# Optimization experiments

Hardware: AMD Instinct MI355X
Metric: run time of the kernel (lower is better)

## Reference

```python
import jax, jax.numpy as jnp
import numpy as np

B, T, C, H = 2, 2048, 1024, 16
N = C // H
TM_DIM, TD_DIM = 32, 64
EPS = 1e-5 * 8 ** 2  # GroupNorm eps from the module


def setup_inputs() -> dict:
    key = jax.random.key(0)
    ks = jax.random.split(key, 16)
    nrm = lambda k, shp, s: jax.random.normal(k, shp, dtype=jnp.float32) * s
    uni = lambda k, shp, a: jax.random.uniform(k, shp, jnp.float32, -a, a)
    ddd = (jnp.arange(C, dtype=jnp.float32) / C).reshape(1, 1, C)
    return {
        "x": nrm(ks[0], (B, T, C), 1.0),
        "time_maa_x": 1.0 - ddd ** 0.5,
        "time_maa_w": 1.0 - ddd ** 0.5,
        "time_maa_k": 1.0 - ddd ** 0.5,
        "time_maa_v": 1.0 - (ddd ** 0.5 + 0.15),
        "time_maa_r": 1.0 - ddd ** 0.25,
        "time_maa_g": 1.0 - ddd ** 0.25,
        "time_maa_w1": uni(ks[1], (C, 5 * TM_DIM), 1e-4),
        "time_maa_w2": uni(ks[2], (5, TM_DIM, C), 1e-4),
        "time_decay": jnp.linspace(-6.0, -1.0, C).astype(jnp.float32).reshape(1, 1, C),
        "time_decay_w1": uni(ks[3], (C, TD_DIM), 1e-4),
        "time_decay_w2": uni(ks[4], (TD_DIM, C), 1e-4),
        "time_faaaa": nrm(ks[5], (H, N), 0.1),
        "W_r": nrm(ks[6], (C, C), C ** -0.5),
        "W_k": nrm(ks[7], (C, C), C ** -0.5),
        "W_v": nrm(ks[8], (C, C), C ** -0.5),
        "W_g": nrm(ks[9], (C, C), C ** -0.5),
        "W_o": nrm(ks[10], (C, C), C ** -0.5),
        "ln_w": jnp.ones((C,), jnp.float32),
        "ln_b": jnp.zeros((C,), jnp.float32),
    }


def _forward(x, tmx, tmw, tmk, tmv, tmr, tmg, maa_w1, maa_w2, tdecay, td_w1,
             td_w2, u, Wr, Wk, Wv, Wg, Wo, ln_w, ln_b):
    Bq, Tq, Cq = x.shape
    # time_shift: x[t-1] with zero at t=0
    xx = jnp.concatenate([jnp.zeros_like(x[:, :1]), x[:, :-1]], axis=1) - x
    xxx = x + xx * tmx
    t5 = jnp.tanh(xxx @ maa_w1).reshape(Bq, Tq, 5, TM_DIM)
    m = jnp.einsum('btfe,fec->fbtc', t5, maa_w2)  # [5,B,T,C] data-dependent mix
    xw = x + xx * (tmw + m[0])
    xk = x + xx * (tmk + m[1])
    xv = x + xx * (tmv + m[2])
    xr = x + xx * (tmr + m[3])
    xg = x + xx * (tmg + m[4])
    r = xr @ Wr
    k = xk @ Wk
    v = xv @ Wv
    g = jax.nn.silu(xg @ Wg)
    w = tdecay + jnp.tanh(xw @ td_w1) @ td_w2          # [B,T,C] log-log decay
    decay = jnp.exp(-jnp.exp(w))                        # in (0,1)
    to_tbhn = lambda a: a.reshape(Bq, Tq, H, N).transpose(1, 0, 2, 3)
    rT, kT, vT, dT = (to_tbhn(a) for a in (r, k, v, decay))

    def step(S, inp):  # S: [B,H,N,N] (key_dim i, value_dim j)
        r_t, k_t, v_t, d_t = inp
        kv = k_t[..., :, None] * v_t[..., None, :]
        y = jnp.einsum('bhi,bhij->bhj', r_t, S + u[None, :, :, None] * kv)
        return d_t[..., None] * S + kv, y

    S0 = jnp.zeros((Bq, H, N, N), x.dtype)
    _, ys = jax.lax.scan(step, S0, (rT, kT, vT, dT))
    y = ys.transpose(1, 0, 2, 3).reshape(Bq, Tq, Cq)
    # GroupNorm with H groups over channels
    yh = y.reshape(Bq, Tq, H, N)
    mu = yh.mean(-1, keepdims=True)
    var = yh.var(-1, keepdims=True)
    yn = (yh - mu) / jnp.sqrt(var + EPS)
    yn = (yn * ln_w.reshape(H, N) + ln_b.reshape(H, N)).reshape(Bq, Tq, Cq)
    return (yn * g) @ Wo


def reference(x, time_maa_x, time_maa_w, time_maa_k, time_maa_v, time_maa_r,
              time_maa_g, time_maa_w1, time_maa_w2, time_decay, time_decay_w1,
              time_decay_w2, time_faaaa, W_r, W_k, W_v, W_g, W_o, ln_w, ln_b):
    return _forward(x, time_maa_x, time_maa_w, time_maa_k, time_maa_v,
                    time_maa_r, time_maa_g, time_maa_w1, time_maa_w2,
                    time_decay, time_decay_w1, time_decay_w2, time_faaaa,
                    W_r, W_k, W_v, W_g, W_o, ln_w, ln_b)
```

## Files before the change

kernel.cpp:

```cpp
#include <hip/hip_runtime.h>
#include <hip/hip_bf16.h>
#include <cstdint>
#include <cstddef>

#define B_ 2
#define T_ 2048
#define C_ 1024
#define H_ 16
#define NCH 32
#define CHL 64

typedef unsigned short ushort_t;
typedef __bf16 bf16x8 __attribute__((ext_vector_type(8)));
typedef float f32x4 __attribute__((ext_vector_type(4)));

__device__ __forceinline__ ushort_t f2bf(float f) {
  union { float f; uint32_t u; } x; x.f = f;
  uint32_t r = x.u + 0x7fffu + ((x.u >> 16) & 1u);
  return (ushort_t)(r >> 16);
}
__device__ __forceinline__ float bf2f(ushort_t h) {
  union { uint32_t u; float f; } x; x.u = (uint32_t)h << 16; return x.f;
}

__device__ __forceinline__ void gload16(const void* g, void* l) {
  __builtin_amdgcn_global_load_lds(
      (const __attribute__((address_space(1))) void*)g,
      (__attribute__((address_space(3))) void*)l, 16, 0, 0);
}

#define FENCE() asm volatile("" ::: "memory")
#define BAR() do { FENCE(); __builtin_amdgcn_s_barrier(); FENCE(); } while (0)

__device__ __forceinline__ void stb(ushort_t* tile, int row, int col, ushort_t v) {
  *(ushort_t*)((char*)tile + row * 128 + ((col * 2) ^ ((row & 7) << 4))) = v;
}
__device__ __forceinline__ bf16x8 ldb(const ushort_t* tile, int row, int kbyte) {
  return *(const bf16x8*)((const char*)tile + row * 128 + (kbyte ^ ((row & 7) << 4)));
}

struct TDesc { const float* src; ushort_t* dst; int R, Cc, Cpad; };
struct TArgs { TDesc d[9]; };

__global__ __launch_bounds__(256) void transpose_cvt(TArgs args) {
  TDesc D = args.d[blockIdx.z];
  int c0 = blockIdx.x * 32, r0 = blockIdx.y * 32;
  if (c0 >= D.Cpad || r0 >= D.R) return;
  __shared__ float tile[32][33];
  int tx = threadIdx.x & 31, ty = threadIdx.x >> 5;
#pragma unroll
  for (int i = 0; i < 32; i += 8) {
    int r = r0 + ty + i, c = c0 + tx;
    tile[ty + i][tx] = (r < D.R && c < D.Cc) ? D.src[(size_t)r * D.Cc + c] : 0.f;
  }
  __syncthreads();
#pragma unroll
  for (int i = 0; i < 32; i += 8) {
    int c = c0 + ty + i, r = r0 + tx;
    if (c < D.Cpad && r < D.R) D.dst[(size_t)c * D.R + r] = f2bf(tile[tx][ty + i]);
  }
}

__global__ __launch_bounds__(256) void prep_kernel(
    const float* __restrict__ x, const float* __restrict__ tmx,
    float* __restrict__ xx, ushort_t* __restrict__ xxx) {
  size_t idx = ((size_t)blockIdx.x * 256 + threadIdx.x) * 4;
  int tt = (int)((idx >> 10) & (T_ - 1));
  int c = (int)(idx & (C_ - 1));
  float4 xv = *(const float4*)&x[idx];
  float4 xp;
  if (tt == 0) { xp.x = xp.y = xp.z = xp.w = 0.f; }
  else xp = *(const float4*)&x[idx - C_];
  float4 tm = *(const float4*)&tmx[c];
  float4 d;
  d.x = xp.x - xv.x; d.y = xp.y - xv.y; d.z = xp.z - xv.z; d.w = xp.w - xv.w;
  *(float4*)&xx[idx] = d;
  xxx[idx + 0] = f2bf(xv.x + d.x * tm.x);
  xxx[idx + 1] = f2bf(xv.y + d.y * tm.y);
  xxx[idx + 2] = f2bf(xv.z + d.z * tm.z);
  xxx[idx + 3] = f2bf(xv.w + d.w * tm.w);
}

template <int EPI>
__global__ __launch_bounds__(256) void gemm_bt(
    const ushort_t* __restrict__ A, int lda,
    const ushort_t* __restrict__ Bt, int ldb,
    void* __restrict__ Cp, int ldc, int K,
    const float* __restrict__ aux2) {
  __shared__ ushort_t sA[128 * 32];
  __shared__ ushort_t sB[128 * 32];
  const int t = threadIdx.x;
  const int l = t & 63;
  const int w = t >> 6;
  const int wm = w >> 1, wn = w & 1;
  const int m0 = blockIdx.x * 128, n0 = blockIdx.y * 128;
  const int lr = l & 15;
  const int lk = (l >> 4) * 8;

  f32x4 acc[4][4] = {};

  for (int kt = 0; kt < K; kt += 32) {
    __syncthreads();
#pragma unroll
    for (int it = 0; it < 2; ++it) {
      int cbase = it * 256 + w * 64;
      int ca = cbase + l;
      int row = ca >> 2, kc = ca & 3;
      gload16(A + (size_t)(m0 + row) * lda + kt + kc * 8, (char*)sA + (size_t)cbase * 16);
      gload16(Bt + (size_t)(n0 + row) * ldb + kt + kc * 8, (char*)sB + (size_t)cbase * 16);
    }
    __syncthreads();
    bf16x8 af[4], bfr[4];
#pragma unroll
    for (int mi = 0; mi < 4; ++mi)
      af[mi] = *(const bf16x8*)&sA[(wm * 64 + mi * 16 + lr) * 32 + lk];
#pragma unroll
    for (int ni = 0; ni < 4; ++ni)
      bfr[ni] = *(const bf16x8*)&sB[(wn * 64 + ni * 16 + lr) * 32 + lk];
#pragma unroll
    for (int mi = 0; mi < 4; ++mi)
#pragma unroll
      for (int ni = 0; ni < 4; ++ni)
        acc[mi][ni] = __builtin_amdgcn_mfma_f32_16x16x32_bf16(af[mi], bfr[ni], acc[mi][ni], 0, 0, 0);
  }
#pragma unroll
  for (int mi = 0; mi < 4; ++mi) {
#pragma unroll
    for (int ni = 0; ni < 4; ++ni) {
      int col = n0 + wn * 64 + ni * 16 + lr;
#pragma unroll
      for (int r = 0; r < 4; ++r) {
        int row = m0 + wm * 64 + mi * 16 + (l >> 4) * 4 + r;
        float v = acc[mi][ni][r];
        size_t idx = (size_t)row * ldc + col;
        if constexpr (EPI == 4) {
          ((float*)Cp)[idx] = __expf(aux2[col] + v);
        } else {
          ((float*)Cp)[idx] = v;
        }
      }
    }
  }
}

__global__ __launch_bounds__(256) void gemm_bt32(
    const ushort_t* __restrict__ A, int lda,
    const ushort_t* __restrict__ Bt, int ldb,
    ushort_t* __restrict__ Cp, int ldc, int K) {
  __shared__ ushort_t sA[32 * 32];
  __shared__ ushort_t sB[128 * 32];
  const int t = threadIdx.x;
  const int l = t & 63;
  const int w = t >> 6;
  const int m0 = blockIdx.x * 32, n0 = blockIdx.y * 128;
  const int lr = l & 15, lk = (l >> 4) * 8;

  f32x4 acc[2][2] = {};
  for (int kt = 0; kt < K; kt += 32) {
    __syncthreads();
    if (t < 128) {
      int row = t >> 2, kc = t & 3;
      gload16(A + (size_t)(m0 + row) * lda + kt + kc * 8, (char*)sA + t * 16);
    }
#pragma unroll
    for (int it = 0; it < 2; ++it) {
      int ca = it * 256 + t;
      int row = ca >> 2, kc = ca & 3;
      gload16(Bt + (size_t)(n0 + row) * ldb + kt + kc * 8,
              (char*)sB + it * 4096 + w * 1024);
    }
    __syncthreads();
    bf16x8 af[2], bfr[2];
#pragma unroll
    for (int mi = 0; mi < 2; ++mi)
      af[mi] = *(const bf16x8*)&sA[(mi * 16 + lr) * 32 + lk];
#pragma unroll
    for (int ni = 0; ni < 2; ++ni)
      bfr[ni] = *(const bf16x8*)&sB[(w * 32 + ni * 16 + lr) * 32 + lk];
#pragma unroll
    for (int mi = 0; mi < 2; ++mi)
#pragma unroll
      for (int ni = 0; ni < 2; ++ni)
        acc[mi][ni] = __builtin_amdgcn_mfma_f32_16x16x32_bf16(af[mi], bfr[ni], acc[mi][ni], 0, 0, 0);
  }
#pragma unroll
  for (int mi = 0; mi < 2; ++mi)
#pragma unroll
    for (int ni = 0; ni < 2; ++ni) {
      int col = n0 + w * 32 + ni * 16 + lr;
#pragma unroll
      for (int r = 0; r < 4; ++r) {
        int row = m0 + mi * 16 + (l >> 4) * 4 + r;
        Cp[(size_t)row * ldc + col] = f2bf(tanhf(acc[mi][ni][r]));
      }
    }
}

struct PDesc { const ushort_t* A; const ushort_t* Bt; void* C; int epi; };
struct PArgs { PDesc d[4]; };

__global__ __launch_bounds__(512, 1) void gemm_proj256(PArgs args) {
  PDesc D = args.d[blockIdx.z];
  __shared__ ushort_t sMem[2][2][4][4096];
  const int tid = threadIdx.x;
  const int w = tid >> 6, l = tid & 63;
  const int wm = w >> 2, wn = w & 3;
  const int lr = l & 15, hi4 = l >> 4;
  const int m0 = blockIdx.x * 256, n0 = blockIdx.y * 256;

  const int srow = tid >> 3;
  const int scol = (((tid & 7) ^ (srow & 7)) << 3);
  const ushort_t* Abase = D.A + (size_t)(m0 + srow) * C_ + scol;
  const ushort_t* Bbase = D.Bt + (size_t)(n0 + srow) * C_ + scol;
  const int dst16 = tid * 16;

  f32x4 acc[8][4] = {};
  bf16x8 bfr[2][4];

#define STG_A(db, unit, kt) \
  gload16(Abase + (size_t)(unit) * 64 * C_ + (kt), (char*)&sMem[db][0][unit][0] + dst16)
#define STG_B(db, unit, kt) \
  gload16(Bbase + (size_t)(unit) * 64 * C_ + (kt), (char*)&sMem[db][1][unit][0] + dst16)

#define LDA_(b, p, i, kk)                                                      \
  (*(const bf16x8*)((const char*)&sMem[b][0][wm * 2 + ((p) >> 1)][0] +         \
                    (((2 * (p) + (i)) & 3) * 16 + lr) * 128 +                  \
                    ((((kk)*4 + hi4) ^ (lr & 7)) << 4)))
#define LDB_(b, ni, kk)                                                        \
  (*(const bf16x8*)((const char*)&sMem[b][1][wn][0] +                          \
                    ((ni)*16 + lr) * 128 + ((((kk)*4 + hi4) ^ (lr & 7)) << 4)))

#define PH(b, p, STAGES, VM)                                                   \
  do {                                                                         \
    bf16x8 a00, a10, a01, a11;                                                 \
    if ((p) == 0) {                                                            \
      _Pragma("unroll") for (int kk = 0; kk < 2; ++kk)                         \
      _Pragma("unroll") for (int ni = 0; ni < 4; ++ni)                         \
        bfr[kk][ni] = LDB_(b, ni, kk);                                         \
    }                                                                          \
    a00 = LDA_(b, p, 0, 0); a10 = LDA_(b, p, 1, 0);                            \
    a01 = LDA_(b, p, 0, 1); a11 = LDA_(b, p, 1, 1);                            \
    STAGES;                                                                    \
    VM;                                                                        \
    BAR();                                                                     \
    asm volatile("s_waitcnt lgkmcnt(0)" ::: "memory");                         \
    __builtin_amdgcn_sched_barrier(0);                                         \
    __builtin_amdgcn_s_setprio(1);                                             \
    _Pragma("unroll") for (int ni = 0; ni < 4; ++ni) {                         \
      acc[2 * (p)][ni] = __builtin_amdgcn_mfma_f32_16x16x32_bf16(              \
          a00, bfr[0][ni], acc[2 * (p)][ni], 0, 0, 0);                         \
      acc[2 * (p) + 1][ni] = __builtin_amdgcn_mfma_f32_16x16x32_bf16(          \
          a10, bfr[0][ni], acc[2 * (p) + 1][ni], 0, 0, 0);                     \
      acc[2 * (p)][ni] = __builtin_amdgcn_mfma_f32_16x16x32_bf16(              \
          a01, bfr[1][ni], acc[2 * (p)][ni], 0, 0, 0);                         \
      acc[2 * (p) + 1][ni] = __builtin_amdgcn_mfma_f32_16x16x32_bf16(          \
          a11, bfr[1][ni], acc[2 * (p) + 1][ni], 0, 0, 0);                     \
    }                                                                          \
    __builtin_amdgcn_s_setprio(0);                                             \
    BAR();                                                                     \
  } while (0)

#define TILE(b, kt1, kt2)                                                      \
  do {                                                                         \
    PH(b, 0, { STG_A((b) ^ 1, 1, kt1); STG_A((b) ^ 1, 3, kt1); }, );           \
    PH(b, 1, { STG_B(b, 0, kt2); STG_B(b, 1, kt2); },                          \
       asm volatile("s_waitcnt vmcnt(10)" ::: "memory"));                      \
    PH(b, 2, { STG_B(b, 2, kt2); STG_B(b, 3, kt2); }, );                       \
    PH(b, 3, { STG_A(b, 0, kt2); STG_A(b, 2, kt2); },                          \
       asm volatile("s_waitcnt vmcnt(8)" ::: "memory"));                       \
  } while (0)

  STG_B(0, 0, 0);  STG_B(0, 1, 0);
  STG_B(0, 2, 0);  STG_B(0, 3, 0);
  STG_A(0, 0, 0);  STG_A(0, 2, 0);
  STG_A(0, 1, 0);  STG_A(0, 3, 0);
  STG_B(1, 0, 64); STG_B(1, 1, 64);
  STG_B(1, 2, 64); STG_B(1, 3, 64);
  STG_A(1, 0, 64); STG_A(1, 2, 64);
  asm volatile("s_waitcnt vmcnt(8)" ::: "memory");
  BAR();

#pragma unroll 1
  for (int j = 0; j < 16; j += 2) {
    int ka1 = ((j + 1) & 15) * 64, ka2 = ((j + 2) & 15) * 64;
    int kb1 = ((j + 2) & 15) * 64, kb2 = ((j + 3) & 15) * 64;
    TILE(0, ka1, ka2);
    TILE(1, kb1, kb2);
  }
  asm volatile("s_waitcnt vmcnt(0)" ::: "memory");

  const int epi = D.epi;
#pragma unroll
  for (int mi = 0; mi < 8; ++mi)
#pragma unroll
    for (int ni = 0; ni < 4; ++ni) {
      int col = n0 + wn * 64 + ni * 16 + lr;
#pragma unroll
      for (int r = 0; r < 4; ++r) {
        int row = m0 + wm * 128 + mi * 16 + hi4 * 4 + r;
        float v = acc[mi][ni][r];
        size_t idx = (size_t)row * C_ + col;
        if (epi == 2) {
          v = v / (1.f + __expf(-v));
          ((ushort_t*)D.C)[idx] = f2bf(v);
        } else {
          ((float*)D.C)[idx] = v;
        }
      }
    }
#undef TILE
#undef PH
#undef LDB_
#undef LDA_
#undef STG_B
#undef STG_A
}

struct MixArgs { const float* tm[5]; ushort_t* dst[5]; };

__global__ __launch_bounds__(256) void fused_mix(
    const float* __restrict__ x, const float* __restrict__ xx,
    const ushort_t* __restrict__ t5, const ushort_t* __restrict__ w2t,
    MixArgs margs) {
  __shared__ float xs[64 * 128];
  __shared__ float xxs[64 * 128];
  __shared__ ushort_t sA[64 * 32];
  __shared__ ushort_t sB[128 * 32];
  const int t = threadIdx.x;
  const int l = t & 63;
  const int w = t >> 6;
  const int wm = w >> 1, wn = w & 1;
  const int m0 = blockIdx.x * 64, n0 = blockIdx.y * 128;
  const int lr = l & 15;
  const int lk = (l >> 4) * 8;

#pragma unroll
  for (int it = 0; it < 8; ++it) {
    int row = it * 8 + (t >> 5);
    int c16 = t & 31;
    gload16(x + (size_t)(m0 + row) * C_ + n0 + c16 * 4, (char*)xs + row * 512 + c16 * 16);
    gload16(xx + (size_t)(m0 + row) * C_ + n0 + c16 * 4, (char*)xxs + row * 512 + c16 * 16);
  }

  for (int f = 0; f < 5; ++f) {
    __syncthreads();
    {
      int row = t >> 2, c8 = t & 3;
      gload16(t5 + (size_t)(m0 + row) * 256 + f * 32 + c8 * 8, (char*)sA + t * 16);
    }
#pragma unroll
    for (int it = 0; it < 2; ++it) {
      int row = it * 64 + (t >> 2), c8 = t & 3;
      gload16(w2t + (size_t)(n0 + row) * 160 + f * 32 + c8 * 8,
              (char*)sB + it * 4096 + t * 16);
    }
    __syncthreads();
    bf16x8 af[2], bfr[4];
#pragma unroll
    for (int mi = 0; mi < 2; ++mi)
      af[mi] = *(const bf16x8*)&sA[(wm * 32 + mi * 16 + lr) * 32 + lk];
#pragma unroll
    for (int ni = 0; ni < 4; ++ni)
      bfr[ni] = *(const bf16x8*)&sB[(wn * 64 + ni * 16 + lr) * 32 + lk];
    f32x4 acc[2][4] = {};
#pragma unroll
    for (int mi = 0; mi < 2; ++mi)
#pragma unroll
      for (int ni = 0; ni < 4; ++ni)
        acc[mi][ni] = __builtin_amdgcn_mfma_f32_16x16x32_bf16(af[mi], bfr[ni], acc[mi][ni], 0, 0, 0);
    const float* tmf = margs.tm[f];
    ushort_t* dst = margs.dst[f];
#pragma unroll
    for (int mi = 0; mi < 2; ++mi) {
#pragma unroll
      for (int ni = 0; ni < 4; ++ni) {
        int cl = wn * 64 + ni * 16 + lr;
        int col = n0 + cl;
        float tmv = tmf[col];
#pragma unroll
        for (int r = 0; r < 4; ++r) {
          int rl = wm * 32 + mi * 16 + (l >> 4) * 4 + r;
          int row = m0 + rl;
          float xv = xs[rl * 128 + cl];
          float xxv = xxs[rl * 128 + cl];
          dst[(size_t)row * C_ + col] = f2bf(xv + xxv * (tmv + acc[mi][ni][r]));
        }
      }
    }
  }
}

__global__ __launch_bounds__(256) void chunk_local(
    const float* __restrict__ rx, const float* __restrict__ kx,
    const float* __restrict__ vx, const float* __restrict__ lamx,
    const float* __restrict__ u, float* __restrict__ Mt,
    float* __restrict__ aLg, ushort_t* __restrict__ rAg,
    float* __restrict__ yo) {
  int c = blockIdx.x, bh = blockIdx.y;
  int b = bh >> 4, h = bh & 15;
  __shared__ ushort_t sRA[64 * 64], sKA[64 * 64], sKh[64 * 64], sKl[64 * 64],
                      sVh[64 * 64], sVl[64 * 64], sP[64 * 64];
  __shared__ float qsum[4][64];
  __shared__ float ruk[64];
  const int tid = threadIdx.x;
  const int i = tid & 63;
  const int q = tid >> 6;
  size_t base = ((size_t)b * T_ + (size_t)c * CHL) * C_ + h * 64;
  size_t cb = ((size_t)c * 32 + bh);

  float lam[16];
  float run = 0.f;
#pragma unroll
  for (int s = 0; s < 16; ++s) {
    lam[s] = lamx[base + (size_t)(q * 16 + s) * C_ + i];
    run += lam[s];
  }
  qsum[q][i] = run;
  __syncthreads();
  float pre = 0.f, ct = 0.f;
#pragma unroll
  for (int qq = 0; qq < 4; ++qq) {
    float vq = qsum[qq][i];
    ct += vq;
    if (qq < q) pre += vq;
  }
  float uu = u[h * 64 + i];
  float ci = pre;
#pragma unroll
  for (int s = 0; s < 16; ++s) {
    int t = q * 16 + s;
    ci += lam[s];
    float cl = ci - lam[s];
    size_t o = base + (size_t)t * C_ + i;
    float rv = rx[o], kv = kx[o], vv = vx[o];
    ushort_t ra = f2bf(rv * __expf(-cl));
    stb(sRA, t, i, ra);
    rAg[cb * 4096 + t * 64 + i] = ra;
    stb(sKA, t, i, f2bf(kv * __expf(ci)));
    float kal = kv * __expf(ci - ct);
    ushort_t khv = f2bf(kal);
    stb(sKh, i, t, khv);
    stb(sKl, i, t, f2bf(kal - bf2f(khv)));
    ushort_t vhv = f2bf(vv);
    stb(sVh, i, t, vhv);
    stb(sVl, i, t, f2bf(vv - bf2f(vhv)));
    float rr = rv * uu * kv;
#pragma unroll
    for (int m = 32; m; m >>= 1) rr += __shfl_xor(rr, m);
    if (i == 0) ruk[t] = rr;
  }
  if (q == 0) aLg[cb * 64 + i] = __expf(-ct);
  __syncthreads();

  const int l = tid & 63, w = tid >> 6;
  const int wm = w >> 1, wn = w & 1;
  const int lr = l & 15, hi4 = l >> 4;

  {
    f32x4 accP[2][2] = {};
#pragma unroll
    for (int kk = 0; kk < 2; ++kk) {
      bf16x8 af[2], bf_[2];
#pragma unroll
      for (int mi = 0; mi < 2; ++mi) af[mi] = ldb(sRA, wm * 32 + mi * 16 + lr, kk * 64 + hi4 * 16);
#pragma unroll
      for (int ni = 0; ni < 2; ++ni) bf_[ni] = ldb(sKA, wn * 32 + ni * 16 + lr, kk * 64 + hi4 * 16);
#pragma unroll
      for (int mi = 0; mi < 2; ++mi)
#pragma unroll
        for (int ni = 0; ni < 2; ++ni)
          accP[mi][ni] = __builtin_amdgcn_mfma_f32_16x16x32_bf16(af[mi], bf_[ni], accP[mi][ni], 0, 0, 0);
    }
#pragma unroll
    for (int mi = 0; mi < 2; ++mi)
#pragma unroll
      for (int ni = 0; ni < 2; ++ni)
#pragma unroll
        for (int r = 0; r < 4; ++r) {
          int tl = wm * 32 + mi * 16 + hi4 * 4 + r, sl = wn * 32 + ni * 16 + lr;
          float v = accP[mi][ni][r];
          v = sl < tl ? v : (sl == tl ? ruk[tl] : 0.f);
          stb(sP, tl, sl, f2bf(v));
        }
  }
  __syncthreads();

  f32x4 accY[2][2] = {}, accM[2][2] = {};
#pragma unroll
  for (int kk = 0; kk < 2; ++kk) {
    bf16x8 pa[2], vhA[2], vlA[2], vhB[2], vlB[2], khB[2], klB[2];
#pragma unroll
    for (int mi = 0; mi < 2; ++mi) {
      int rw = wm * 32 + mi * 16 + lr;
      pa[mi] = ldb(sP, rw, kk * 64 + hi4 * 16);
      vhA[mi] = ldb(sVh, rw, kk * 64 + hi4 * 16);
      vlA[mi] = ldb(sVl, rw, kk * 64 + hi4 * 16);
    }
#pragma unroll
    for (int ni = 0; ni < 2; ++ni) {
      int rw = wn * 32 + ni * 16 + lr;
      vhB[ni] = ldb(sVh, rw, kk * 64 + hi4 * 16);
      vlB[ni] = ldb(sVl, rw, kk * 64 + hi4 * 16);
      khB[ni] = ldb(sKh, rw, kk * 64 + hi4 * 16);
      klB[ni] = ldb(sKl, rw, kk * 64 + hi4 * 16);
    }
#pragma unroll
    for (int mi = 0; mi < 2; ++mi)
#pragma unroll
      for (int ni = 0; ni < 2; ++ni) {
        accY[mi][ni] = __builtin_amdgcn_mfma_f32_16x16x32_bf16(pa[mi], vhB[ni], accY[mi][ni], 0, 0, 0);
        accY[mi][ni] = __builtin_amdgcn_mfma_f32_16x16x32_bf16(pa[mi], vlB[ni], accY[mi][ni], 0, 0, 0);
        accM[mi][ni] = __builtin_amdgcn_mfma_f32_16x16x32_bf16(vhA[mi], khB[ni], accM[mi][ni], 0, 0, 0);
        accM[mi][ni] = __builtin_amdgcn_mfma_f32_16x16x32_bf16(vhA[mi], klB[ni], accM[mi][ni], 0, 0, 0);
        accM[mi][ni] = __builtin_amdgcn_mfma_f32_16x16x32_bf16(vlA[mi], khB[ni], accM[mi][ni], 0, 0, 0);
      }
  }
#pragma unroll
  for (int mi = 0; mi < 2; ++mi)
#pragma unroll
    for (int ni = 0; ni < 2; ++ni)
#pragma unroll
      for (int r = 0; r < 4; ++r) {
        int rw = wm * 32 + mi * 16 + hi4 * 4 + r;
        int cw = wn * 32 + ni * 16 + lr;
        yo[base + (size_t)rw * C_ + cw] = accY[mi][ni][r];
        Mt[cb * 4096 + rw * 64 + cw] = accM[mi][ni][r];
      }
}

__global__ __launch_bounds__(256) void combine2(
    const float* __restrict__ Mt, const float* __restrict__ aLg,
    ushort_t* __restrict__ S0h, ushort_t* __restrict__ S0l) {
  int bh = blockIdx.x >> 2;
  int ij = ((blockIdx.x & 3) * 256 + threadIdx.x) * 4;
  int i = ij & 63;
  float4 s = {0.f, 0.f, 0.f, 0.f};
  for (int c = 0; c < NCH; ++c) {
    size_t o = ((size_t)c * 32 + bh) * 4096 + ij;
    float4 m = *(const float4*)&Mt[o];
    float4 p = *(const float4*)&aLg[((size_t)c * 32 + bh) * 64 + i];
    ushort4 hi, lo;
    hi.x = f2bf(s.x); lo.x = f2bf(s.x - bf2f(hi.x));
    hi.y = f2bf(s.y); lo.y = f2bf(s.y - bf2f(hi.y));
    hi.z = f2bf(s.z); lo.z = f2bf(s.z - bf2f(hi.z));
    hi.w = f2bf(s.w); lo.w = f2bf(s.w - bf2f(hi.w));
    *(ushort4*)&S0h[o] = hi;
    *(ushort4*)&S0l[o] = lo;
    s.x = p.x * s.x + m.x; s.y = p.y * s.y + m.y;
    s.z = p.z * s.z + m.z; s.w = p.w * s.w + m.w;
  }
}

__global__ __launch_bounds__(256) void inter_gn(
    const ushort_t* __restrict__ rAg, const ushort_t* __restrict__ S0h,
    const ushort_t* __restrict__ S0l, const float* __restrict__ yin,
    const ushort_t* __restrict__ gx, const float* __restrict__ lnw,
    const float* __restrict__ lnb, ushort_t* __restrict__ Z) {
  int c = blockIdx.x, bh = blockIdx.y;
  int b = bh >> 4, h = bh & 15;
  __shared__ ushort_t sRA[64 * 64], sSh[64 * 64], sSl[64 * 64];
  __shared__ float st[64][2][2];
  const int tid = threadIdx.x;
  size_t cb = ((size_t)c * 32 + bh) * 4096;
#pragma unroll
  for (int it = 0; it < 2; ++it) {
    int lb = tid * 32 + it * 16;
    int row = lb >> 7, wi = lb & 127;
    int so = row * 128 + (wi ^ ((row & 7) << 4));
    *(uint4*)((char*)sRA + so) = *(const uint4*)((const char*)(rAg + cb) + lb);
    *(uint4*)((char*)sSh + so) = *(const uint4*)((const char*)(S0h + cb) + lb);
    *(uint4*)((char*)sSl + so) = *(const uint4*)((const char*)(S0l + cb) + lb);
  }
  const int l = tid & 63, w = tid >> 6;
  const int wm = w >> 1, wn = w & 1;
  const int lr = l & 15, hi4 = l >> 4;
  size_t base = ((size_t)b * T_ + (size_t)c * CHL) * C_ + h * 64;

  f32x4 acc[2][2];
#pragma unroll
  for (int mi = 0; mi < 2; ++mi)
#pragma unroll
    for (int ni = 0; ni < 2; ++ni)
#pragma unroll
      for (int r = 0; r < 4; ++r)
        acc[mi][ni][r] = yin[base + (size_t)(wm * 32 + mi * 16 + hi4 * 4 + r) * C_ +
                             wn * 32 + ni * 16 + lr];
  __syncthreads();
#pragma unroll
  for (int kk = 0; kk < 2; ++kk) {
    bf16x8 af[2], bh_[2], bl_[2];
#pragma unroll
    for (int mi = 0; mi < 2; ++mi) af[mi] = ldb(sRA, wm * 32 + mi * 16 + lr, kk * 64 + hi4 * 16);
#pragma unroll
    for (int ni = 0; ni < 2; ++ni) {
      bh_[ni] = ldb(sSh, wn * 32 + ni * 16 + lr, kk * 64 + hi4 * 16);
      bl_[ni] = ldb(sSl, wn * 32 + ni * 16 + lr, kk * 64 + hi4 * 16);
    }
#pragma unroll
    for (int mi = 0; mi < 2; ++mi)
#pragma unroll
      for (int ni = 0; ni < 2; ++ni) {
        acc[mi][ni] = __builtin_amdgcn_mfma_f32_16x16x32_bf16(af[mi], bh_[ni], acc[mi][ni], 0, 0, 0);
        acc[mi][ni] = __builtin_amdgcn_mfma_f32_16x16x32_bf16(af[mi], bl_[ni], acc[mi][ni], 0, 0, 0);
      }
  }
#pragma unroll
  for (int mi = 0; mi < 2; ++mi)
#pragma unroll
    for (int r = 0; r < 4; ++r) {
      int row = wm * 32 + mi * 16 + hi4 * 4 + r;
      float s1 = acc[mi][0][r] + acc[mi][1][r];
      float s2 = acc[mi][0][r] * acc[mi][0][r] + acc[mi][1][r] * acc[mi][1][r];
#pragma unroll
      for (int m = 1; m < 16; m <<= 1) { s1 += __shfl_xor(s1, m); s2 += __shfl_xor(s2, m); }
      if (lr == 0) { st[row][wn][0] = s1; st[row][wn][1] = s2; }
    }
  __syncthreads();
#pragma unroll
  for (int mi = 0; mi < 2; ++mi)
#pragma unroll
    for (int ni = 0; ni < 2; ++ni)
#pragma unroll
      for (int r = 0; r < 4; ++r) {
        int row = wm * 32 + mi * 16 + hi4 * 4 + r;
        int jl = wn * 32 + ni * 16 + lr;
        float S1 = st[row][0][0] + st[row][1][0];
        float S2 = st[row][0][1] + st[row][1][1];
        float mu = S1 * (1.f / 64.f);
        float var = S2 * (1.f / 64.f) - mu * mu;
        float rs = rsqrtf(var + 6.4e-4f);
        int col = h * 64 + jl;
        size_t o = base + (size_t)row * C_ + jl;
        float yn = (acc[mi][ni][r] - mu) * rs * lnw[col] + lnb[col];
        Z[o] = f2bf(yn * bf2f(gx[o]));
      }
}

extern "C" void kernel_launch(void* const* d_in, const int* in_sizes, int n_in,
                              void* d_out, int out_size, void* d_ws, size_t ws_size,
                              hipStream_t stream) {
  const float* x    = (const float*)d_in[0];
  const float* tmx  = (const float*)d_in[1];
  const float* tmw  = (const float*)d_in[2];
  const float* tmk  = (const float*)d_in[3];
  const float* tmv  = (const float*)d_in[4];
  const float* tmr  = (const float*)d_in[5];
  const float* tmg  = (const float*)d_in[6];
  const float* maaw1 = (const float*)d_in[7];
  const float* maaw2 = (const float*)d_in[8];
  const float* tdec = (const float*)d_in[9];
  const float* tdw1 = (const float*)d_in[10];
  const float* tdw2 = (const float*)d_in[11];
  const float* u    = (const float*)d_in[12];
  const float* Wr   = (const float*)d_in[13];
  const float* Wk   = (const float*)d_in[14];
  const float* Wv   = (const float*)d_in[15];
  const float* Wg   = (const float*)d_in[16];
  const float* Wo   = (const float*)d_in[17];
  const float* lnw  = (const float*)d_in[18];
  const float* lnb  = (const float*)d_in[19];

  char* ws = (char*)d_ws;
  const size_t MB = 1ull << 20;
  float*    xx     = (float*)(ws + 0);
  ushort_t* xxx    = (ushort_t*)(ws + 16 * MB);
  ushort_t* WrT    = (ushort_t*)(ws + 24 * MB);
  ushort_t* WkT    = (ushort_t*)(ws + 26 * MB);
  ushort_t* WvT    = (ushort_t*)(ws + 28 * MB);
  ushort_t* WgT    = (ushort_t*)(ws + 30 * MB);
  ushort_t* WoT    = (ushort_t*)(ws + 32 * MB);
  ushort_t* maaW1T = (ushort_t*)(ws + 34 * MB);
  ushort_t* tdW1T  = (ushort_t*)(ws + 35 * MB);
  ushort_t* tdW2T  = (ushort_t*)(ws + 35 * MB + 256 * 1024);
  ushort_t* maaW2T = (ushort_t*)(ws + 35 * MB + 512 * 1024);
  ushort_t* t5     = (ushort_t*)(ws + 36 * MB);
  ushort_t* t5d    = (ushort_t*)(ws + 38 * MB);
  ushort_t* Xm[5];
  for (int f = 0; f < 5; ++f) Xm[f] = (ushort_t*)(ws + 40 * MB + (size_t)f * 8 * MB);
  float*    Mtb = (float*)(ws + 40 * MB);
  ushort_t* S0h = (ushort_t*)(ws + 56 * MB);
  ushort_t* S0l = (ushort_t*)(ws + 64 * MB);
  ushort_t* rAg = (ushort_t*)(ws + 72 * MB);
  float* rb   = (float*)(ws + 80 * MB);
  float* kb   = (float*)(ws + 96 * MB);
  float* vb   = (float*)(ws + 112 * MB);
  ushort_t* gbh = (ushort_t*)(ws + 128 * MB);
  float* lam  = (float*)(ws + 144 * MB);
  float* aLg  = (float*)(ws + 160 * MB);
  float* yb   = (float*)(ws + 0);
  ushort_t* Zb = (ushort_t*)(ws + 16 * MB);

  TArgs ta;
  ta.d[0] = TDesc{Wr,    WrT,    1024, 1024, 1024};
  ta.d[1] = TDesc{Wk,    WkT,    1024, 1024, 1024};
  ta.d[2] = TDesc{Wv,    WvT,    1024, 1024, 1024};
  ta.d[3] = TDesc{Wg,    WgT,    1024, 1024, 1024};
  ta.d[4] = TDesc{Wo,    WoT,    1024, 1024, 1024};
  ta.d[5] = TDesc{maaw1, maaW1T, 1024, 160,  256};
  ta.d[6] = TDesc{tdw1,  tdW1T,  1024, 64,   128};
  ta.d[7] = TDesc{tdw2,  tdW2T,  64,   1024, 1024};
  ta.d[8] = TDesc{maaw2, maaW2T, 160,  1024, 1024};
  transpose_cvt<<<dim3(32, 32, 9), 256, 0, stream>>>(ta);

  prep_kernel<<<(B_ * T_ * C_) / 1024, 256, 0, stream>>>(x, tmx, xx, xxx);

  gemm_bt32<<<dim3(128, 2), 256, 0, stream>>>(xxx, C_, maaW1T, C_, t5, 256, C_);

  MixArgs ma;
  ma.tm[0] = tmw; ma.tm[1] = tmk; ma.tm[2] = tmv; ma.tm[3] = tmr; ma.tm[4] = tmg;
  for (int f = 0; f < 5; ++f) ma.dst[f] = Xm[f];
  fused_mix<<<dim3(64, 8), 256, 0, stream>>>(x, xx, t5, maaW2T, ma);

  PArgs pa;
  pa.d[0] = PDesc{Xm[3], WrT, rb, 0};
  pa.d[1] = PDesc{Xm[1], WkT, kb, 0};
  pa.d[2] = PDesc{Xm[2], WvT, vb, 0};
  pa.d[3] = PDesc{Xm[4], WgT, gbh, 2};
  gemm_proj256<<<dim3(16, 4, 4), 512, 0, stream>>>(pa);

  gemm_bt32<<<dim3(128, 1), 256, 0, stream>>>(Xm[0], C_, tdW1T, C_, t5d, 128, C_);
  gemm_bt<4><<<dim3(32, 8), 256, 0, stream>>>(t5d, 128, tdW2T, 64, lam, C_, 64, tdec);

  chunk_local<<<dim3(NCH, B_ * H_), 256, 0, stream>>>(rb, kb, vb, lam, u, Mtb, aLg, rAg, yb);
  combine2<<<128, 256, 0, stream>>>(Mtb, aLg, S0h, S0l);
  inter_gn<<<dim3(NCH, B_ * H_), 256, 0, stream>>>(rAg, S0h, S0l, yb, gbh, lnw, lnb, Zb);

  PArgs po;
  po.d[0] = PDesc{Zb, WoT, d_out, 0};
  po.d[1] = po.d[0]; po.d[2] = po.d[0]; po.d[3] = po.d[0];
  gemm_proj256<<<dim3(16, 4, 1), 512, 0, stream>>>(po);
}
```

Measured before the change: 205.1 us.

## Store r projection in bf16, software-pipeline combine2, use gemm_bt for output

The r projection now writes bf16 through a new epilogue mode, and chunk_local reads it as bf16. This halves that buffer's write and read traffic at the cost of some precision on r. combine2 now runs as 256 blocks of 128 threads and prefetches the next chunk's Mt and aLg values so load latency overlaps the serial recurrence. The final output projection switches from gemm_proj256 with a single descriptor to the gemm_bt<0> kernel with a different grid.

```diff
diff --git a/kernel.cpp b/kernel.cpp
--- a/kernel.cpp
+++ b/kernel.cpp
@@ -303,6 +303,8 @@
         if (epi == 2) {
           v = v / (1.f + __expf(-v));
           ((ushort_t*)D.C)[idx] = f2bf(v);
+        } else if (epi == 3) {
+          ((ushort_t*)D.C)[idx] = f2bf(v);
         } else {
           ((float*)D.C)[idx] = v;
         }
@@ -391,7 +393,7 @@
 }
 
 __global__ __launch_bounds__(256) void chunk_local(
-    const float* __restrict__ rx, const float* __restrict__ kx,
+    const ushort_t* __restrict__ rxh, const float* __restrict__ kx,
     const float* __restrict__ vx, const float* __restrict__ lamx,
     const float* __restrict__ u, float* __restrict__ Mt,
     float* __restrict__ aLg, ushort_t* __restrict__ rAg,
@@ -432,7 +434,7 @@
     ci += lam[s];
     float cl = ci - lam[s];
     size_t o = base + (size_t)t * C_ + i;
-    float rv = rx[o], kv = kx[o], vv = vx[o];
+    float rv = bf2f(rxh[o]), kv = kx[o], vv = vx[o];
     ushort_t ra = f2bf(rv * __expf(-cl));
     stb(sRA, t, i, ra);
     rAg[cb * 4096 + t * 64 + i] = ra;
@@ -528,26 +530,36 @@
       }
 }
 
-__global__ __launch_bounds__(256) void combine2(
+__global__ __launch_bounds__(128) void combine2(
     const float* __restrict__ Mt, const float* __restrict__ aLg,
     ushort_t* __restrict__ S0h, ushort_t* __restrict__ S0l) {
-  int bh = blockIdx.x >> 2;
-  int ij = ((blockIdx.x & 3) * 256 + threadIdx.x) * 4;
+  int bh = blockIdx.x >> 3;
+  int ij = ((blockIdx.x & 7) * 128 + threadIdx.x) * 4;
   int i = ij & 63;
+  const float* Mp = Mt + (size_t)bh * 4096 + ij;
+  const float* Pp = aLg + (size_t)bh * 64 + i;
+  ushort_t* Hp = S0h + (size_t)bh * 4096 + ij;
+  ushort_t* Lp = S0l + (size_t)bh * 4096 + ij;
   float4 s = {0.f, 0.f, 0.f, 0.f};
+  float4 m = *(const float4*)Mp;
+  float4 p = *(const float4*)Pp;
   for (int c = 0; c < NCH; ++c) {
-    size_t o = ((size_t)c * 32 + bh) * 4096 + ij;
-    float4 m = *(const float4*)&Mt[o];
-    float4 p = *(const float4*)&aLg[((size_t)c * 32 + bh) * 64 + i];
+    float4 mn, pn;
+    if (c < NCH - 1) {
+      mn = *(const float4*)(Mp + (size_t)(c + 1) * (32 * 4096));
+      pn = *(const float4*)(Pp + (size_t)(c + 1) * (32 * 64));
+    }
+    size_t o = (size_t)c * (32 * 4096);
     ushort4 hi, lo;
     hi.x = f2bf(s.x); lo.x = f2bf(s.x - bf2f(hi.x));
     hi.y = f2bf(s.y); lo.y = f2bf(s.y - bf2f(hi.y));
     hi.z = f2bf(s.z); lo.z = f2bf(s.z - bf2f(hi.z));
     hi.w = f2bf(s.w); lo.w = f2bf(s.w - bf2f(hi.w));
-    *(ushort4*)&S0h[o] = hi;
-    *(ushort4*)&S0l[o] = lo;
+    *(ushort4*)(Hp + o) = hi;
+    *(ushort4*)(Lp + o) = lo;
     s.x = p.x * s.x + m.x; s.y = p.y * s.y + m.y;
     s.z = p.z * s.z + m.z; s.w = p.w * s.w + m.w;
+    m = mn; p = pn;
   }
 }
 
@@ -681,7 +693,7 @@
   ushort_t* S0h = (ushort_t*)(ws + 56 * MB);
   ushort_t* S0l = (ushort_t*)(ws + 64 * MB);
   ushort_t* rAg = (ushort_t*)(ws + 72 * MB);
-  float* rb   = (float*)(ws + 80 * MB);
+  ushort_t* rbh = (ushort_t*)(ws + 80 * MB);
   float* kb   = (float*)(ws + 96 * MB);
   float* vb   = (float*)(ws + 112 * MB);
   ushort_t* gbh = (ushort_t*)(ws + 128 * MB);
@@ -712,7 +724,7 @@
   fused_mix<<<dim3(64, 8), 256, 0, stream>>>(x, xx, t5, maaW2T, ma);
 
   PArgs pa;
-  pa.d[0] = PDesc{Xm[3], WrT, rb, 0};
+  pa.d[0] = PDesc{Xm[3], WrT, rbh, 3};
   pa.d[1] = PDesc{Xm[1], WkT, kb, 0};
   pa.d[2] = PDesc{Xm[2], WvT, vb, 0};
   pa.d[3] = PDesc{Xm[4], WgT, gbh, 2};
@@ -721,12 +733,9 @@
   gemm_bt32<<<dim3(128, 1), 256, 0, stream>>>(Xm[0], C_, tdW1T, C_, t5d, 128, C_);
   gemm_bt<4><<<dim3(32, 8), 256, 0, stream>>>(t5d, 128, tdW2T, 64, lam, C_, 64, tdec);
 
-  chunk_local<<<dim3(NCH, B_ * H_), 256, 0, stream>>>(rb, kb, vb, lam, u, Mtb, aLg, rAg, yb);
-  combine2<<<128, 256, 0, stream>>>(Mtb, aLg, S0h, S0l);
+  chunk_local<<<dim3(NCH, B_ * H_), 256, 0, stream>>>(rbh, kb, vb, lam, u, Mtb, aLg, rAg, yb);
+  combine2<<<256, 128, 0, stream>>>(Mtb, aLg, S0h, S0l);
   inter_gn<<<dim3(NCH, B_ * H_), 256, 0, stream>>>(rAg, S0h, S0l, yb, gbh, lnw, lnb, Zb);
 
-  PArgs po;
-  po.d[0] = PDesc{Zb, WoT, d_out, 0};
-  po.d[1] = po.d[0]; po.d[2] = po.d[0]; po.d[3] = po.d[0];
-  gemm_proj256<<<dim3(16, 4, 1), 512, 0, stream>>>(po);
-}
+  gemm_bt<0><<<dim3(32, 8), 256, 0, stream>>>(Zb, C_, WoT, C_, (float*)d_out, C_, C_, nullptr);
+}
```

New measurement: 207.0 us. No clear change (+0.9%).
